# Kernel tuning notes

Measured on AMD Instinct MI355X. Metric: run time of the kernel, lower is better.

The kernel has to match this reference:

```python
import jax, jax.numpy as jnp
import numpy as np

# ---- static config (eval-mode RPN, torchvision-style FPN) ----
LEVEL_HW = [(200, 200), (100, 100), (50, 50), (25, 25), (13, 13)]
STRIDES = [4, 8, 16, 32, 64]
SIZES = [32, 64, 128, 256, 512]
A = 3                      # anchors per location (3 aspect ratios)
IMG_H, IMG_W = 800, 800
PRE_N, POST_N = 1000, 1000 # pre/post NMS top-n (testing)
NMS_TH, SCORE_TH, MIN_SIZE = 0.7, 0.0, 1e-3
BBOX_CLIP = 4.135166556742356  # log(1000/16), BoxCoder clamp
NUM_PER_LEVEL = [A * h * w for h, w in LEVEL_HW]


def _make_anchors():
    ratios = np.array([0.5, 1.0, 2.0])
    hr = np.sqrt(ratios)
    wr = 1.0 / hr
    out = []
    for (H, W), size, stride in zip(LEVEL_HW, SIZES, STRIDES):
        ws, hs = wr * size, hr * size
        base = np.stack([-ws / 2, -hs / 2, ws / 2, hs / 2], axis=1)  # [A,4]
        sx = np.arange(W) * stride
        sy = np.arange(H) * stride
        yy, xx = np.meshgrid(sy, sx, indexing='ij')
        shifts = np.stack([xx.ravel(), yy.ravel(), xx.ravel(), yy.ravel()], axis=1)
        out.append((shifts[:, None, :] + base[None, :, :]).reshape(-1, 4))
    return np.concatenate(out, 0).astype(np.float32)


def setup_inputs() -> dict:
    key = jax.random.key(0)
    ks = jax.random.split(key, 10)
    N = 4
    inp = {}
    for i, (h, w) in enumerate(LEVEL_HW):
        inp[f'obj{i}'] = jax.random.normal(ks[i], (N, A, h, w), jnp.float32)
        inp[f'delta{i}'] = 0.5 * jax.random.normal(ks[5 + i], (N, 4 * A, h, w), jnp.float32)
    inp['anchors'] = jnp.asarray(_make_anchors())
    return inp


def _decode(deltas, anchors):
    # BoxCoder.decode with weights (1,1,1,1)
    wa = anchors[:, 2] - anchors[:, 0]
    ha = anchors[:, 3] - anchors[:, 1]
    cxa = anchors[:, 0] + 0.5 * wa
    cya = anchors[:, 1] + 0.5 * ha
    dx, dy = deltas[..., 0], deltas[..., 1]
    dw = jnp.minimum(deltas[..., 2], BBOX_CLIP)
    dh = jnp.minimum(deltas[..., 3], BBOX_CLIP)
    cx = dx * wa + cxa
    cy = dy * ha + cya
    w = jnp.exp(dw) * wa
    h = jnp.exp(dh) * ha
    return jnp.stack([cx - 0.5 * w, cy - 0.5 * h, cx + 0.5 * w, cy + 0.5 * h], -1)


def _box_iou(b1, b2):
    a1 = (b1[:, 2] - b1[:, 0]) * (b1[:, 3] - b1[:, 1])
    a2 = (b2[:, 2] - b2[:, 0]) * (b2[:, 3] - b2[:, 1])
    lt = jnp.maximum(b1[:, None, :2], b2[None, :, :2])
    rb = jnp.minimum(b1[:, None, 2:], b2[None, :, 2:])
    wh = jnp.clip(rb - lt, 0.0)
    inter = wh[..., 0] * wh[..., 1]
    return inter / (a1[:, None] + a2[None, :] - inter)


def _nms_keep(iou, valid):
    # greedy NMS over score-sorted boxes; valid marks surviving pre-filters
    K = iou.shape[0]
    def body(sup, i):
        k = valid[i] & jnp.logical_not(sup[i])
        sup = sup | (k & (iou[i] > NMS_TH))
        return sup, k
    _, keeps = jax.lax.scan(body, jnp.zeros(K, bool), jnp.arange(K))
    return keeps


def _per_image(boxes, scores, lvl):
    # clip_boxes_to_image
    x1 = jnp.clip(boxes[:, 0], 0.0, IMG_W)
    y1 = jnp.clip(boxes[:, 1], 0.0, IMG_H)
    x2 = jnp.clip(boxes[:, 2], 0.0, IMG_W)
    y2 = jnp.clip(boxes[:, 3], 0.0, IMG_H)
    boxes = jnp.stack([x1, y1, x2, y2], -1)
    # remove_small_boxes + score_thresh as validity mask
    valid = (x2 - x1 >= MIN_SIZE) & (y2 - y1 >= MIN_SIZE) & (scores >= SCORE_TH)
    ms = jnp.where(valid, scores, -1.0)
    order = jnp.argsort(-ms)
    b_s, v_s, s_s, l_s = boxes[order], valid[order], scores[order], lvl[order]
    # batched_nms trick: offset boxes by level so levels never overlap
    bn = jax.lax.stop_gradient(b_s) + (l_s.astype(boxes.dtype) * (IMG_W + 1.0))[:, None]
    keep = _nms_keep(_box_iou(bn, bn), v_s)
    sel_key = jnp.where(keep, jax.lax.stop_gradient(s_s), -1.0)
    topv, topi = jax.lax.top_k(sel_key, POST_N)
    m = topv > -0.5
    fb = jnp.where(m[:, None], b_s[topi], 0.0)
    fs = jnp.where(m, s_s[topi], 0.0)
    return fb, fs


def reference(obj0, obj1, obj2, obj3, obj4, delta0, delta1, delta2, delta3, delta4, anchors):
    objs = [obj0, obj1, obj2, obj3, obj4]
    dels = [delta0, delta1, delta2, delta3, delta4]
    N = obj0.shape[0]
    # permute_and_flatten + concat (objectness C=1)
    obj = jnp.concatenate([o.transpose(0, 2, 3, 1).reshape(N, -1) for o in objs], 1)
    dl = jnp.concatenate([
        d.reshape(N, A, 4, d.shape[2], d.shape[3]).transpose(0, 3, 4, 1, 2).reshape(N, -1, 4)
        for d in dels], 1)
    proposals = _decode(dl, anchors)  # [N, total, 4]
    levels = jnp.concatenate([jnp.full((n,), i, jnp.int32) for i, n in enumerate(NUM_PER_LEVEL)])
    # per-level top-k (static split)
    idxs, off = [], 0
    for n in NUM_PER_LEVEL:
        k = min(PRE_N, n)
        _, ti = jax.lax.top_k(obj[:, off:off + n], k)
        idxs.append(ti + off)
        off += n
    top_idx = jnp.concatenate(idxs, 1)  # [N, K]
    sel_obj = jnp.take_along_axis(obj, top_idx, 1)
    sel_lvl = levels[top_idx]
    sel_box = jnp.take_along_axis(proposals, top_idx[..., None], 1)
    scores = jax.nn.sigmoid(sel_obj)
    fb, fs = jax.vmap(_per_image)(sel_box, scores, sel_lvl)
    return fb, fs
```

## Files before the change

kernel.cpp:

```cpp
#include <hip/hip_runtime.h>
#include <cstdint>
#include <cstddef>

#define NLV 5
#define NIMG 4
#define NSEL 4507
#define TSEL (NIMG * NSEL)
#define POSTN 1000
#define TCAP 8192
#define TTCAP 2048
#define NHB 16
#define PBLK 64
#define PCH 1875

__device__ const int d_W[NLV]    = {200, 100, 50, 25, 13};
__device__ const int d_NL[NLV]   = {120000, 30000, 7500, 1875, 507};
__device__ const int d_KOFF[6]   = {0, 120000, 150000, 157500, 159375, 159882};
__device__ const int d_LOFF[6]   = {0, 1000, 2000, 3000, 4000, 4507};
__device__ const int d_KL[NLV]   = {1000, 1000, 1000, 1000, 507};

struct Ptrs {
    const float* obj[NLV];
    const float* del[NLV];
    const float* anch;
};

__device__ inline unsigned int dkey_of(float f) {
    unsigned int u = __float_as_uint(f);
    unsigned int mk = (u & 0x80000000u) ? ~u : (u | 0x80000000u);
    return ~mk;
}
__device__ inline float logit_from_dkey(unsigned int dk) {
    unsigned int mk = ~dk;
    unsigned int u = (mk & 0x80000000u) ? (mk & 0x7fffffffu) : ~mk;
    return __uint_as_float(u);
}

__global__ __launch_bounds__(256) void k_hist(Ptrs P, unsigned int* hist) {
    int l = blockIdx.y, n = blockIdx.z;
    int nl_sz = d_NL[l];
    if (d_KL[l] >= nl_sz) return;
    int nlid = n * NLV + l;
    __shared__ unsigned int h[2048];
    for (int i = threadIdx.x; i < 2048; i += 256) h[i] = 0;
    __syncthreads();
    const float* ob = P.obj[l] + (size_t)n * nl_sz;
    int chunk = (nl_sz + NHB - 1) / NHB;
    int beg = blockIdx.x * chunk;
    int end = min(beg + chunk, nl_sz);
    for (int t = beg + (int)threadIdx.x; t < end; t += 256)
        atomicAdd(&h[dkey_of(ob[t]) >> 21], 1u);
    __syncthreads();
    unsigned int* out = hist + ((size_t)nlid * NHB + blockIdx.x) * 2048;
    for (int i = threadIdx.x; i < 2048; i += 256) out[i] = h[i];
}

__global__ __launch_bounds__(1024) void k_thresh(const unsigned int* hist,
                                                 unsigned int* thr,
                                                 int* scnt, int* tcnt) {
    int nlid = blockIdx.x;
    int l = nlid % NLV;
    if (threadIdx.x == 0) { scnt[nlid] = 0; tcnt[nlid] = 0; }
    if (d_KL[l] >= d_NL[l]) return;
    int tid = threadIdx.x, w = tid >> 6, lane = tid & 63;
    __shared__ unsigned int wpre[16];
    const unsigned int* hb = hist + (size_t)nlid * NHB * 2048;
    unsigned int v0 = 0, v1 = 0;
    #pragma unroll
    for (int sh = 0; sh < NHB; ++sh) {
        v0 += hb[sh * 2048 + 2 * tid];
        v1 += hb[sh * 2048 + 2 * tid + 1];
    }
    unsigned int s = v0 + v1;
    unsigned int ps = s;
    #pragma unroll
    for (int d = 1; d < 64; d <<= 1) {
        unsigned int t2 = (unsigned int)__shfl_up((int)ps, d, 64);
        if (lane >= d) ps += t2;
    }
    if (lane == 63) wpre[w] = ps;
    __syncthreads();
    unsigned int base = 0;
    #pragma unroll
    for (int ww = 0; ww < 16; ++ww) if (ww < w) base += wpre[ww];
    unsigned int incl = base + ps;
    unsigned int target = (unsigned int)d_KL[l];
    unsigned int exc0 = incl - s, inc0 = incl - v1;
    unsigned int exc1 = inc0,    inc1 = incl;
    if (exc0 < target && target <= inc0) { thr[nlid * 2] = 2 * tid;     thr[nlid * 2 + 1] = exc0; }
    if (exc1 < target && target <= inc1) { thr[nlid * 2] = 2 * tid + 1; thr[nlid * 2 + 1] = exc1; }
}

__global__ __launch_bounds__(256) void k_pick(Ptrs P, const unsigned int* thr,
                                              int* scnt, int* tcnt,
                                              int* cg, float* cl,
                                              unsigned long long* tiebuf) {
    int l = blockIdx.y, n = blockIdx.z;
    int nl_sz = d_NL[l], kl = d_KL[l];
    int nlid = n * NLV + l;
    const float* ob = P.obj[l] + (size_t)n * nl_sz;
    int cbase = n * NSEL + d_LOFF[l];
    int koff = d_KOFF[l];
    int Wl = d_W[l], HW = Wl * Wl;
    int chunk = (nl_sz + PBLK - 1) / PBLK;
    int beg = blockIdx.x * chunk;
    int end = min(beg + chunk, nl_sz);
    int tid = threadIdx.x;

    if (kl >= nl_sz) {
        for (int t = beg + tid; t < end; t += 256) {
            int a = t / HW, rem = t - a * HW;
            int p = rem * 3 + a;
            cg[cbase + p] = koff + p;
            cl[cbase + p] = ob[t];
        }
        return;
    }
    __shared__ int sp[PCH];
    __shared__ float sl[PCH];
    __shared__ unsigned long long tb[PCH];
    __shared__ int nsel, ntie, sbase, tbase;
    if (tid == 0) { nsel = 0; ntie = 0; }
    __syncthreads();

    unsigned int b0 = thr[nlid * 2];
    for (int t = beg + tid; t < end; t += 256) {
        float lg = ob[t];
        unsigned int dk = dkey_of(lg);
        unsigned int bin = dk >> 21;
        if (bin < b0) {
            int pos = atomicAdd(&nsel, 1);
            int a = t / HW, rem = t - a * HW;
            sp[pos] = rem * 3 + a;
            sl[pos] = lg;
        } else if (bin == b0) {
            int pos = atomicAdd(&ntie, 1);
            int a = t / HW, rem = t - a * HW;
            tb[pos] = ((unsigned long long)dk << 17) |
                      (unsigned long long)(unsigned int)(rem * 3 + a);
        }
    }
    __syncthreads();
    if (tid == 0) {
        sbase = atomicAdd(&scnt[nlid], nsel);
        tbase = atomicAdd(&tcnt[nlid], ntie);
    }
    __syncthreads();
    int ns = nsel, nt = ntie, sb = sbase, tbs = tbase;
    for (int i = tid; i < ns; i += 256) {
        cg[cbase + sb + i] = koff + sp[i];
        cl[cbase + sb + i] = sl[i];
    }
    for (int i = tid; i < nt; i += 256) {
        int slot = tbs + i;
        if (slot < TCAP) tiebuf[(size_t)nlid * TCAP + slot] = tb[i];
    }
}

__global__ __launch_bounds__(1024) void k_tbs(Ptrs P, const unsigned int* thr,
                                              const int* tcnt,
                                              const unsigned long long* tiebuf,
                                              int* cg, float* cl,
                                              unsigned long long* skey,
                                              float4* sboxL, float* slogL,
                                              int* ccnt) {
#pragma clang fp contract(off)
    __shared__ union {
        struct { unsigned long long kk[TCAP];
                 unsigned long long tt[TTCAP];
                 unsigned int h2[2048]; } tie;
        struct { unsigned long long s[1024];
                 float4 bx[1024];
                 float lg[1024]; } srt;
    } U;
    __shared__ unsigned int wpre[16];
    __shared__ unsigned int s_b1, s_before;
    __shared__ int ctr, ttc;

    int l = blockIdx.x, n = blockIdx.y;
    int nl = n * NLV + l;
    int tid = threadIdx.x, w = tid >> 6, lane = tid & 63;
    int kl = d_KL[l], nl_sz = d_NL[l];
    int cbase = n * NSEL + d_LOFF[l];
    int koff = d_KOFF[l];

    if (kl < nl_sz) {
        int c = min(tcnt[nl], TCAP);
        unsigned int cnt_lt = thr[nl * 2 + 1];
        int need = kl - (int)cnt_lt;
        if (tid == 0) { ctr = 0; ttc = 0; }
        U.tie.h2[tid] = 0; U.tie.h2[tid + 1024] = 0;
        for (int i = tid; i < c; i += 1024) U.tie.kk[i] = tiebuf[(size_t)nl * TCAP + i];
        __syncthreads();
        for (int i = tid; i < c; i += 1024)
            atomicAdd(&U.tie.h2[(unsigned int)((U.tie.kk[i] >> 27) & 0x7ffull)], 1u);
        __syncthreads();
        unsigned int v0 = U.tie.h2[2 * tid], v1 = U.tie.h2[2 * tid + 1];
        unsigned int s = v0 + v1, ps = s;
        #pragma unroll
        for (int d = 1; d < 64; d <<= 1) {
            unsigned int t2 = (unsigned int)__shfl_up((int)ps, d, 64);
            if (lane >= d) ps += t2;
        }
        if (lane == 63) wpre[w] = ps;
        __syncthreads();
        unsigned int base = 0;
        #pragma unroll
        for (int ww = 0; ww < 16; ++ww) if (ww < w) base += wpre[ww];
        unsigned int incl = base + ps;
        unsigned int target = (unsigned int)need;
        unsigned int exc0 = incl - s, inc0 = incl - v1;
        unsigned int exc1 = inc0,    inc1 = incl;
        if (exc0 < target && target <= inc0) { s_b1 = 2 * tid;     s_before = exc0; }
        if (exc1 < target && target <= inc1) { s_b1 = 2 * tid + 1; s_before = exc1; }
        __syncthreads();
        unsigned int b1 = s_b1;
        int before = (int)s_before;
        for (int i = tid; i < c; i += 1024) {
            unsigned long long ki = U.tie.kk[i];
            unsigned int sb = (unsigned int)((ki >> 27) & 0x7ffull);
            if (sb < b1) {
                int slot = atomicAdd(&ctr, 1);
                int p = (int)(ki & 0x1ffffull);
                cg[cbase + (int)cnt_lt + slot] = koff + p;
                cl[cbase + (int)cnt_lt + slot] = logit_from_dkey((unsigned int)(ki >> 17));
            } else if (sb == b1) {
                int j = atomicAdd(&ttc, 1);
                if (j < TTCAP) U.tie.tt[j] = ki;
            }
        }
        __syncthreads();
        int c2 = min(ttc, TTCAP);
        int need2 = need - before;
        for (int i = tid; i < c2; i += 1024) {
            unsigned long long ki = U.tie.tt[i];
            int rank = 0;
            for (int j = 0; j < c2; ++j) rank += (U.tie.tt[j] < ki) ? 1 : 0;
            if (rank < need2) {
                int p = (int)(ki & 0x1ffffull);
                cg[cbase + (int)cnt_lt + before + rank] = koff + p;
                cl[cbase + (int)cnt_lt + before + rank] = logit_from_dkey((unsigned int)(ki >> 17));
            }
        }
    }
    __syncthreads();

    {
        int j = tid;
        unsigned long long key;
        float4 box;
        float lgv;
        if (j >= kl) {
            key = ((unsigned long long)0xFFFFFFFFu << 27) | (unsigned long long)j;
            box = make_float4(0.f, 0.f, 0.f, 0.f);
            lgv = 0.f;
        } else {
            int sidx = cbase + j;
            int gidx = cg[sidx];
            float lg = cl[sidx];
            int p = gidx - koff;
            int Wl = d_W[l];
            int HW = Wl * Wl;
            int a = p % 3, hw = p / 3;
            int hq = hw / Wl, wq = hw - hq * Wl;
            const float* dl = P.del[l];
            size_t dbase = (size_t)(n * 12 + a * 4) * HW + (size_t)hq * Wl + wq;
            float dx = dl[dbase], dy = dl[dbase + HW];
            float dw = dl[dbase + 2 * (size_t)HW], dh = dl[dbase + 3 * (size_t)HW];
            const float* an = P.anch + 4 * (size_t)gidx;
            float ax1 = an[0], ay1 = an[1], ax2 = an[2], ay2 = an[3];
            float wa = ax2 - ax1, ha = ay2 - ay1;
            float cxa = ax1 + 0.5f * wa, cya = ay1 + 0.5f * ha;
            const float CLIPC = (float)4.135166556742356;
            dw = fminf(dw, CLIPC); dh = fminf(dh, CLIPC);
            float cx = dx * wa + cxa;
            float cy = dy * ha + cya;
            float ww2 = expf(dw) * wa;
            float hh2 = expf(dh) * ha;
            float x1 = cx - 0.5f * ww2, y1 = cy - 0.5f * hh2;
            float x2 = cx + 0.5f * ww2, y2 = cy + 0.5f * hh2;
            x1 = fminf(fmaxf(x1, 0.0f), 800.0f);
            y1 = fminf(fmaxf(y1, 0.0f), 800.0f);
            x2 = fminf(fmaxf(x2, 0.0f), 800.0f);
            y2 = fminf(fmaxf(y2, 0.0f), 800.0f);
            bool valid = (x2 - x1 >= 1e-3f) && (y2 - y1 >= 1e-3f);
            box = make_float4(x1, y1, x2, y2);
            lgv = lg;
            unsigned int sk = valid ? dkey_of(lg) : 0xffffffffu;
            key = ((unsigned long long)sk << 27) |
                  ((unsigned long long)(unsigned int)p << 10) | (unsigned long long)j;
        }
        U.srt.s[j] = key;
        U.srt.bx[j] = box;
        U.srt.lg[j] = lgv;
    }
    __syncthreads();

    for (int k = 2; k <= 1024; k <<= 1) {
        for (int j2 = k >> 1; j2 > 0; j2 >>= 1) {
            if (tid < 512) {
                int i = ((tid & ~(j2 - 1)) << 1) | (tid & (j2 - 1));
                int ix = i | j2;
                bool up = ((i & k) == 0);
                unsigned long long A = U.srt.s[i], B = U.srt.s[ix];
                if ((A > B) == up) { U.srt.s[i] = B; U.srt.s[ix] = A; }
            }
            __syncthreads();
        }
    }
    {
        int e = tid;
        unsigned long long key = U.srt.s[e];
        int j = (int)(key & 0x3ffull);
        skey[(size_t)nl * 1024 + e] = key;
        sboxL[(size_t)nl * 1024 + e] = U.srt.bx[j];
        slogL[(size_t)nl * 1024 + e] = U.srt.lg[j];
        bool v = (key >> 27) != 0xFFFFFFFFull;
        bool vn = (e < 1023) ? ((U.srt.s[e + 1] >> 27) != 0xFFFFFFFFull) : false;
        if (e == 0 && !v) ccnt[nl] = 0;
        if (v && (e == 1023 || !vn)) ccnt[nl] = e + 1;
    }
}

__global__ __launch_bounds__(256) void k_mask(const float4* sboxL, const int* ccnt,
                                              unsigned long long* MT) {
#pragma clang fp contract(off)
    int n = blockIdx.z, l = blockIdx.y;
    int ci = blockIdx.x >> 4, cj = blockIdx.x & 15;
    int nl = n * NLV + l;
    int cnt = ccnt[nl];
    int nw = (cnt + 63) / 64;
    if (cj < ci || cj >= nw) return;
    __shared__ float4 bi[64], bj[64];
    int tid = threadIdx.x;
    float off = (float)l * 801.0f;
    if (tid < 64) {
        float4 b = sboxL[nl * 1024 + cj * 64 + tid];
        bj[tid] = make_float4(b.x + off, b.y + off, b.z + off, b.w + off);
    } else if (tid < 128) {
        float4 b = sboxL[nl * 1024 + ci * 64 + (tid - 64)];
        bi[tid - 64] = make_float4(b.x + off, b.y + off, b.z + off, b.w + off);
    }
    __syncthreads();
    int w = tid >> 6, lane = tid & 63;
    float4 B = bj[lane];
    float a2 = (B.z - B.x) * (B.w - B.y);
    unsigned long long* outp = MT + ((size_t)nl * 16 + cj) * 1024 + ci * 64;
    #pragma unroll
    for (int t = 0; t < 16; ++t) {
        int i = w * 16 + t;
        float4 A = bi[i];
        float a1 = (A.z - A.x) * (A.w - A.y);
        float ltx = fmaxf(A.x, B.x), lty = fmaxf(A.y, B.y);
        float rbx = fminf(A.z, B.z), rby = fminf(A.w, B.w);
        float wx = fmaxf(rbx - ltx, 0.f), wy = fmaxf(rby - lty, 0.f);
        float inter = wx * wy;
        float iou = inter / ((a1 + a2) - inter);
        unsigned long long word = __ballot(iou > 0.7f);
        if (lane == 0) outp[i] = word;
    }
}

__global__ __launch_bounds__(1024) void k_scanrank(const unsigned long long* MT,
                                                   const int* ccnt,
                                                   const unsigned long long* skey,
                                                   const float4* sboxL, const float* slogL,
                                                   float* out) {
    int n = blockIdx.x, tid = threadIdx.x, w = tid >> 6, lane = tid & 63;
    __shared__ unsigned long long KS[NLV][1024];
    __shared__ unsigned long long kd[NLV][16];
    __shared__ int kpre[NLV][17];
    __shared__ int lcnt[NLV];
    __shared__ unsigned long long pendS[16];
    __shared__ unsigned long long defS[16];
    for (int i = tid; i < POSTN; i += 1024) {
        ((float4*)out)[n * POSTN + i] = make_float4(0.f, 0.f, 0.f, 0.f);
        out[NIMG * POSTN * 4 + n * POSTN + i] = 0.f;
    }
    for (int e = tid; e < NLV * 1024; e += 1024)
        ((unsigned long long*)KS)[e] = skey[(size_t)n * NLV * 1024 + e];
    if (tid < NLV) lcnt[tid] = ccnt[n * NLV + tid];
    __syncthreads();

    for (int l = 0; l < NLV; ++l) {
        int nl = n * NLV + l;
        int cnt = lcnt[l];
        int nw = (cnt + 63) / 64;
        const unsigned long long* base = MT + ((size_t)nl * 16 + w) * 1024;
        unsigned long long Dmask = 0;
        if (w < nw)
            Dmask = base[(size_t)w * 64 + lane] & ~((2ull << lane) - 1ull);
        unsigned long long rows[15];
        #pragma unroll
        for (int cc = 0; cc < 15; ++cc)
            rows[cc] = (cc < w && w < nw) ? base[(size_t)cc * 64 + lane] : 0ull;

        int nb = max(0, min(64, cnt - w * 64));
        unsigned long long pend_w = (nb == 64) ? ~0ull : ((nb > 0) ? ((1ull << nb) - 1ull) : 0ull);
        unsigned long long K_w = 0;
        if (lane == 0) pendS[w] = pend_w;
        __syncthreads();

        for (int round = 0; round < 1024; ++round) {
            unsigned long long any = 0;
            #pragma unroll
            for (int cc = 0; cc < 16; ++cc) any |= pendS[cc];
            if (!any) break;
            unsigned long long acc = ((pendS[w] >> lane) & 1ull) ? Dmask : 0ull;
            #pragma unroll
            for (int cc = 0; cc < 15; ++cc)
                if (cc < w) acc |= ((pendS[cc] >> lane) & 1ull) ? rows[cc] : 0ull;
            unsigned int vlo = (unsigned int)acc, vhi = (unsigned int)(acc >> 32);
            #pragma unroll
            for (int m = 1; m < 64; m <<= 1) {
                vlo |= (unsigned int)__shfl_xor((int)vlo, m, 64);
                vhi |= (unsigned int)__shfl_xor((int)vhi, m, 64);
            }
            unsigned long long sup = ((unsigned long long)vhi << 32) | (unsigned long long)vlo;
            unsigned long long def_w = pend_w & ~sup;
            K_w |= def_w;
            if (lane == 0) defS[w] = def_w;
            __syncthreads();
            unsigned long long acc2 = ((defS[w] >> lane) & 1ull) ? Dmask : 0ull;
            #pragma unroll
            for (int cc = 0; cc < 15; ++cc)
                if (cc < w) acc2 |= ((defS[cc] >> lane) & 1ull) ? rows[cc] : 0ull;
            unsigned int rlo = (unsigned int)acc2, rhi = (unsigned int)(acc2 >> 32);
            #pragma unroll
            for (int m = 1; m < 64; m <<= 1) {
                rlo |= (unsigned int)__shfl_xor((int)rlo, m, 64);
                rhi |= (unsigned int)__shfl_xor((int)rhi, m, 64);
            }
            unsigned long long rem = ((unsigned long long)rhi << 32) | (unsigned long long)rlo;
            pend_w &= ~def_w & ~rem;
            if (lane == 0) pendS[w] = pend_w;
            __syncthreads();
        }
        if (lane == 0) kd[l][w] = K_w;
        __syncthreads();
    }

    if (tid < NLV) {
        int run = 0;
        for (int q = 0; q < 16; ++q) { kpre[tid][q] = run; run += (int)__popcll(kd[tid][q]); }
        kpre[tid][16] = run;
    }
    __syncthreads();
    for (int e = tid; e < NLV * 1024; e += 1024) {
        int l = e >> 10, i = e & 1023;
        if (i >= lcnt[l]) continue;
        int q = i >> 6, b = i & 63;
        if (!((kd[l][q] >> b) & 1ull)) continue;
        int rank = kpre[l][q] + (int)__popcll(kd[l][q] & ((1ull << b) - 1ull));
        unsigned int sk = (unsigned int)(KS[l][i] >> 27);
        for (int l2 = 0; l2 < NLV; ++l2) {
            if (l2 == l) continue;
            int c2 = lcnt[l2];
            unsigned long long bound = (l2 < l)
                ? (((unsigned long long)sk + 1ull) << 27)
                : ((unsigned long long)sk << 27);
            int lo = 0, hi = c2;
            while (lo < hi) {
                int mid = (lo + hi) >> 1;
                if (KS[l2][mid] < bound) lo = mid + 1; else hi = mid;
            }
            int mq = lo >> 6, mb = lo & 63;
            rank += kpre[l2][mq] + (mb ? (int)__popcll(kd[l2][mq] & ((1ull << mb) - 1ull)) : 0);
        }
        if (rank < POSTN) {
            ((float4*)out)[n * POSTN + rank] = sboxL[(size_t)(n * NLV + l) * 1024 + i];
            float lg = slogL[(size_t)(n * NLV + l) * 1024 + i];
            out[NIMG * POSTN * 4 + n * POSTN + rank] = 1.0f / (1.0f + expf(-lg));
        }
    }
}

extern "C" void kernel_launch(void* const* d_in, const int* in_sizes, int n_in,
                              void* d_out, int out_size, void* d_ws, size_t ws_size,
                              hipStream_t stream) {
    Ptrs P;
    bool interleaved = (in_sizes[1] == 4 * in_sizes[0]);
    for (int i = 0; i < NLV; ++i) {
        if (interleaved) {
            P.obj[i] = (const float*)d_in[2 * i];
            P.del[i] = (const float*)d_in[2 * i + 1];
        } else {
            P.obj[i] = (const float*)d_in[i];
            P.del[i] = (const float*)d_in[NLV + i];
        }
    }
    P.anch = (const float*)d_in[10];

    char* w = (char*)d_ws;
    size_t off = 0;
    auto alloc = [&](size_t bytes) {
        void* p = w + off;
        off = (off + bytes + 255) & ~(size_t)255;
        return p;
    };
    const size_t NLT = (size_t)NIMG * NLV * 1024;
    unsigned int* hist = (unsigned int*)alloc((size_t)NIMG * NLV * NHB * 2048 * 4);
    int* scnt = (int*)alloc(256);
    int* tcnt = (int*)alloc(256);
    unsigned int* thr = (unsigned int*)alloc((size_t)NIMG * NLV * 2 * 4);
    unsigned long long* tiebuf = (unsigned long long*)alloc((size_t)NIMG * NLV * TCAP * 8);
    int* cg      = (int*)alloc((size_t)TSEL * 4);
    float* cl    = (float*)alloc((size_t)TSEL * 4);
    unsigned long long* skey = (unsigned long long*)alloc(NLT * 8);
    float4* sboxL = (float4*)alloc(NLT * 16);
    float* slogL  = (float*)alloc(NLT * 4);
    int* ccnt    = (int*)alloc((size_t)NIMG * NLV * 4);
    unsigned long long* MT = (unsigned long long*)alloc((size_t)NIMG * NLV * 16 * 1024 * 8);
    (void)ws_size; (void)n_in;

    k_hist<<<dim3(NHB, NLV, NIMG), 256, 0, stream>>>(P, hist);
    k_thresh<<<NIMG * NLV, 1024, 0, stream>>>(hist, thr, scnt, tcnt);
    k_pick<<<dim3(PBLK, NLV, NIMG), 256, 0, stream>>>(P, thr, scnt, tcnt, cg, cl, tiebuf);
    k_tbs<<<dim3(NLV, NIMG), 1024, 0, stream>>>(P, thr, tcnt, tiebuf, cg, cl,
                                                skey, sboxL, slogL, ccnt);
    k_mask<<<dim3(256, NLV, NIMG), 256, 0, stream>>>(sboxL, ccnt, MT);
    k_scanrank<<<NIMG, 1024, 0, stream>>>(MT, ccnt, skey, sboxL, slogL, (float*)d_out);
}
```

Before: 190.2 us.

## Split NMS scan and rank into separate kernels parallel over levels

Replaces the single per-image kernel, which ran the five per-level NMS scans one after another, with a scan kernel launched on a (level, image) grid so the 20 level scans run concurrently in separate blocks. The keep bitmasks go to a small global buffer, and a second kernel on the same grid does the cross-level rank computation and scatter. Output zeroing is split across the level blocks, and the zeroing, which now lives in k_scan, runs before k_rank on the same stream. This trades one extra launch and a global round-trip of the keep masks for five times more block-level parallelism in the serial NMS stage.

```diff
diff --git a/kernel.cpp b/kernel.cpp
--- a/kernel.cpp
+++ b/kernel.cpp
@@ -361,117 +361,125 @@
     }
 }
 
-__global__ __launch_bounds__(1024) void k_scanrank(const unsigned long long* MT,
-                                                   const int* ccnt,
-                                                   const unsigned long long* skey,
-                                                   const float4* sboxL, const float* slogL,
-                                                   float* out) {
-    int n = blockIdx.x, tid = threadIdx.x, w = tid >> 6, lane = tid & 63;
+__global__ __launch_bounds__(1024) void k_scan(const unsigned long long* MT,
+                                               const int* ccnt,
+                                               unsigned long long* keepL,
+                                               float* out) {
+    int l = blockIdx.x, n = blockIdx.y;
+    int nl = n * NLV + l;
+    int tid = threadIdx.x, w = tid >> 6, lane = tid & 63;
+    __shared__ unsigned long long pendS[16];
+    __shared__ unsigned long long defS[16];
+    {
+        int seg = POSTN / NLV;
+        for (int i = tid; i < seg; i += 1024) {
+            int idx = n * POSTN + l * seg + i;
+            ((float4*)out)[idx] = make_float4(0.f, 0.f, 0.f, 0.f);
+            out[NIMG * POSTN * 4 + idx] = 0.f;
+        }
+    }
+    int cnt = ccnt[nl];
+    int nw = (cnt + 63) / 64;
+
+    const unsigned long long* base = MT + ((size_t)nl * 16 + w) * 1024;
+    unsigned long long Dmask = 0;
+    if (w < nw)
+        Dmask = base[(size_t)w * 64 + lane] & ~((2ull << lane) - 1ull);
+    unsigned long long rows[15];
+    #pragma unroll
+    for (int cc = 0; cc < 15; ++cc)
+        rows[cc] = (cc < w && w < nw) ? base[(size_t)cc * 64 + lane] : 0ull;
+
+    int nb = max(0, min(64, cnt - w * 64));
+    unsigned long long pend_w = (nb == 64) ? ~0ull : ((nb > 0) ? ((1ull << nb) - 1ull) : 0ull);
+    unsigned long long K_w = 0;
+    if (lane == 0) pendS[w] = pend_w;
+    __syncthreads();
+
+    for (int round = 0; round < 1024; ++round) {
+        unsigned long long any = 0;
+        #pragma unroll
+        for (int cc = 0; cc < 16; ++cc) any |= pendS[cc];
+        if (!any) break;
+        unsigned long long acc = ((pendS[w] >> lane) & 1ull) ? Dmask : 0ull;
+        #pragma unroll
+        for (int cc = 0; cc < 15; ++cc)
+            if (cc < w) acc |= ((pendS[cc] >> lane) & 1ull) ? rows[cc] : 0ull;
+        unsigned int vlo = (unsigned int)acc, vhi = (unsigned int)(acc >> 32);
+        #pragma unroll
+        for (int m = 1; m < 64; m <<= 1) {
+            vlo |= (unsigned int)__shfl_xor((int)vlo, m, 64);
+            vhi |= (unsigned int)__shfl_xor((int)vhi, m, 64);
+        }
+        unsigned long long sup = ((unsigned long long)vhi << 32) | (unsigned long long)vlo;
+        unsigned long long def_w = pend_w & ~sup;
+        K_w |= def_w;
+        if (lane == 0) defS[w] = def_w;
+        __syncthreads();
+        unsigned long long acc2 = ((defS[w] >> lane) & 1ull) ? Dmask : 0ull;
+        #pragma unroll
+        for (int cc = 0; cc < 15; ++cc)
+            if (cc < w) acc2 |= ((defS[cc] >> lane) & 1ull) ? rows[cc] : 0ull;
+        unsigned int rlo = (unsigned int)acc2, rhi = (unsigned int)(acc2 >> 32);
+        #pragma unroll
+        for (int m = 1; m < 64; m <<= 1) {
+            rlo |= (unsigned int)__shfl_xor((int)rlo, m, 64);
+            rhi |= (unsigned int)__shfl_xor((int)rhi, m, 64);
+        }
+        unsigned long long rem = ((unsigned long long)rhi << 32) | (unsigned long long)rlo;
+        pend_w &= ~def_w & ~rem;
+        if (lane == 0) pendS[w] = pend_w;
+        __syncthreads();
+    }
+    if (lane == 0) keepL[nl * 16 + w] = K_w;
+}
+
+__global__ __launch_bounds__(1024) void k_rank(const unsigned long long* skey,
+                                               const unsigned long long* keepL,
+                                               const int* ccnt,
+                                               const float4* sboxL, const float* slogL,
+                                               float* out) {
+    int l = blockIdx.x, n = blockIdx.y;
+    int tid = threadIdx.x;
     __shared__ unsigned long long KS[NLV][1024];
     __shared__ unsigned long long kd[NLV][16];
     __shared__ int kpre[NLV][17];
     __shared__ int lcnt[NLV];
-    __shared__ unsigned long long pendS[16];
-    __shared__ unsigned long long defS[16];
-    for (int i = tid; i < POSTN; i += 1024) {
-        ((float4*)out)[n * POSTN + i] = make_float4(0.f, 0.f, 0.f, 0.f);
-        out[NIMG * POSTN * 4 + n * POSTN + i] = 0.f;
-    }
     for (int e = tid; e < NLV * 1024; e += 1024)
         ((unsigned long long*)KS)[e] = skey[(size_t)n * NLV * 1024 + e];
+    if (tid < NLV * 16) ((unsigned long long*)kd)[tid] = keepL[n * NLV * 16 + tid];
     if (tid < NLV) lcnt[tid] = ccnt[n * NLV + tid];
     __syncthreads();
-
-    for (int l = 0; l < NLV; ++l) {
-        int nl = n * NLV + l;
-        int cnt = lcnt[l];
-        int nw = (cnt + 63) / 64;
-        const unsigned long long* base = MT + ((size_t)nl * 16 + w) * 1024;
-        unsigned long long Dmask = 0;
-        if (w < nw)
-            Dmask = base[(size_t)w * 64 + lane] & ~((2ull << lane) - 1ull);
-        unsigned long long rows[15];
-        #pragma unroll
-        for (int cc = 0; cc < 15; ++cc)
-            rows[cc] = (cc < w && w < nw) ? base[(size_t)cc * 64 + lane] : 0ull;
-
-        int nb = max(0, min(64, cnt - w * 64));
-        unsigned long long pend_w = (nb == 64) ? ~0ull : ((nb > 0) ? ((1ull << nb) - 1ull) : 0ull);
-        unsigned long long K_w = 0;
-        if (lane == 0) pendS[w] = pend_w;
-        __syncthreads();
-
-        for (int round = 0; round < 1024; ++round) {
-            unsigned long long any = 0;
-            #pragma unroll
-            for (int cc = 0; cc < 16; ++cc) any |= pendS[cc];
-            if (!any) break;
-            unsigned long long acc = ((pendS[w] >> lane) & 1ull) ? Dmask : 0ull;
-            #pragma unroll
-            for (int cc = 0; cc < 15; ++cc)
-                if (cc < w) acc |= ((pendS[cc] >> lane) & 1ull) ? rows[cc] : 0ull;
-            unsigned int vlo = (unsigned int)acc, vhi = (unsigned int)(acc >> 32);
-            #pragma unroll
-            for (int m = 1; m < 64; m <<= 1) {
-                vlo |= (unsigned int)__shfl_xor((int)vlo, m, 64);
-                vhi |= (unsigned int)__shfl_xor((int)vhi, m, 64);
-            }
-            unsigned long long sup = ((unsigned long long)vhi << 32) | (unsigned long long)vlo;
-            unsigned long long def_w = pend_w & ~sup;
-            K_w |= def_w;
-            if (lane == 0) defS[w] = def_w;
-            __syncthreads();
-            unsigned long long acc2 = ((defS[w] >> lane) & 1ull) ? Dmask : 0ull;
-            #pragma unroll
-            for (int cc = 0; cc < 15; ++cc)
-                if (cc < w) acc2 |= ((defS[cc] >> lane) & 1ull) ? rows[cc] : 0ull;
-            unsigned int rlo = (unsigned int)acc2, rhi = (unsigned int)(acc2 >> 32);
-            #pragma unroll
-            for (int m = 1; m < 64; m <<= 1) {
-                rlo |= (unsigned int)__shfl_xor((int)rlo, m, 64);
-                rhi |= (unsigned int)__shfl_xor((int)rhi, m, 64);
-            }
-            unsigned long long rem = ((unsigned long long)rhi << 32) | (unsigned long long)rlo;
-            pend_w &= ~def_w & ~rem;
-            if (lane == 0) pendS[w] = pend_w;
-            __syncthreads();
-        }
-        if (lane == 0) kd[l][w] = K_w;
-        __syncthreads();
-    }
-
     if (tid < NLV) {
         int run = 0;
         for (int q = 0; q < 16; ++q) { kpre[tid][q] = run; run += (int)__popcll(kd[tid][q]); }
         kpre[tid][16] = run;
     }
     __syncthreads();
-    for (int e = tid; e < NLV * 1024; e += 1024) {
-        int l = e >> 10, i = e & 1023;
-        if (i >= lcnt[l]) continue;
-        int q = i >> 6, b = i & 63;
-        if (!((kd[l][q] >> b) & 1ull)) continue;
-        int rank = kpre[l][q] + (int)__popcll(kd[l][q] & ((1ull << b) - 1ull));
-        unsigned int sk = (unsigned int)(KS[l][i] >> 27);
-        for (int l2 = 0; l2 < NLV; ++l2) {
-            if (l2 == l) continue;
-            int c2 = lcnt[l2];
-            unsigned long long bound = (l2 < l)
-                ? (((unsigned long long)sk + 1ull) << 27)
-                : ((unsigned long long)sk << 27);
-            int lo = 0, hi = c2;
-            while (lo < hi) {
-                int mid = (lo + hi) >> 1;
-                if (KS[l2][mid] < bound) lo = mid + 1; else hi = mid;
-            }
-            int mq = lo >> 6, mb = lo & 63;
-            rank += kpre[l2][mq] + (mb ? (int)__popcll(kd[l2][mq] & ((1ull << mb) - 1ull)) : 0);
-        }
-        if (rank < POSTN) {
-            ((float4*)out)[n * POSTN + rank] = sboxL[(size_t)(n * NLV + l) * 1024 + i];
-            float lg = slogL[(size_t)(n * NLV + l) * 1024 + i];
-            out[NIMG * POSTN * 4 + n * POSTN + rank] = 1.0f / (1.0f + expf(-lg));
-        }
+    int i = tid;
+    if (i >= lcnt[l]) return;
+    int q = i >> 6, b = i & 63;
+    if (!((kd[l][q] >> b) & 1ull)) return;
+    int rank = kpre[l][q] + (int)__popcll(kd[l][q] & ((1ull << b) - 1ull));
+    unsigned int sk = (unsigned int)(KS[l][i] >> 27);
+    for (int l2 = 0; l2 < NLV; ++l2) {
+        if (l2 == l) continue;
+        int c2 = lcnt[l2];
+        unsigned long long bound = (l2 < l)
+            ? (((unsigned long long)sk + 1ull) << 27)
+            : ((unsigned long long)sk << 27);
+        int lo = 0, hi = c2;
+        while (lo < hi) {
+            int mid = (lo + hi) >> 1;
+            if (KS[l2][mid] < bound) lo = mid + 1; else hi = mid;
+        }
+        int mq = lo >> 6, mb = lo & 63;
+        rank += kpre[l2][mq] + (mb ? (int)__popcll(kd[l2][mq] & ((1ull << mb) - 1ull)) : 0);
+    }
+    if (rank < POSTN) {
+        ((float4*)out)[n * POSTN + rank] = sboxL[(size_t)(n * NLV + l) * 1024 + i];
+        float lg = slogL[(size_t)(n * NLV + l) * 1024 + i];
+        out[NIMG * POSTN * 4 + n * POSTN + rank] = 1.0f / (1.0f + expf(-lg));
     }
 }
 
@@ -510,6 +518,7 @@
     float4* sboxL = (float4*)alloc(NLT * 16);
     float* slogL  = (float*)alloc(NLT * 4);
     int* ccnt    = (int*)alloc((size_t)NIMG * NLV * 4);
+    unsigned long long* keepL = (unsigned long long*)alloc((size_t)NIMG * NLV * 16 * 8);
     unsigned long long* MT = (unsigned long long*)alloc((size_t)NIMG * NLV * 16 * 1024 * 8);
     (void)ws_size; (void)n_in;
 
@@ -519,5 +528,6 @@
     k_tbs<<<dim3(NLV, NIMG), 1024, 0, stream>>>(P, thr, tcnt, tiebuf, cg, cl,
                                                 skey, sboxL, slogL, ccnt);
     k_mask<<<dim3(256, NLV, NIMG), 256, 0, stream>>>(sboxL, ccnt, MT);
-    k_scanrank<<<NIMG, 1024, 0, stream>>>(MT, ccnt, skey, sboxL, slogL, (float*)d_out);
-}
+    k_scan<<<dim3(NLV, NIMG), 1024, 0, stream>>>(MT, ccnt, keepL, (float*)d_out);
+    k_rank<<<dim3(NLV, NIMG), 1024, 0, stream>>>(skey, keepL, ccnt, sboxL, slogL, (float*)d_out);
+}
```

After: 159.7 us. -16.0%, faster.
